# Kernel optimization log

Measured on AMD Instinct MI355X. Metric: run time of the kernel, lower is better.

Reference implementation:

```python
import jax, jax.numpy as jnp
import numpy as np

NUM_HEADS = 16
HIDDEN = 1024
TOTAL = 2048
NSEG = 8


def setup_inputs() -> dict:
    key = jax.random.key(0)
    ks = jax.random.split(key, 10)
    x = jax.random.normal(ks[0], (TOTAL, HIDDEN), dtype=jnp.float32)
    # cu_seqlens: [0, b1, ..., TOTAL], sorted segment boundaries
    inner = np.sort(np.random.default_rng(0).integers(1, TOTAL, size=NSEG - 1))
    cu_seqlens = jnp.asarray(np.concatenate([[0], inner, [TOTAL]]), dtype=jnp.int32)
    s = 1.0 / np.sqrt(HIDDEN)
    def lin(k):
        kw, kb = jax.random.split(k)
        W = jax.random.uniform(kw, (HIDDEN, HIDDEN), jnp.float32, -s, s)
        b = jax.random.uniform(kb, (HIDDEN,), jnp.float32, -s, s)
        return W, b
    Wq, bq = lin(ks[1]); Wk, bk = lin(ks[2]); Wv, bv = lin(ks[3]); Wo, bo = lin(ks[4])
    return {"hidden_states_packed": x, "cu_seqlens": cu_seqlens,
            "Wq": Wq, "bq": bq, "Wk": Wk, "bk": bk,
            "Wv": Wv, "bv": bv, "Wo": Wo, "bo": bo}


def reference(hidden_states_packed, cu_seqlens, Wq, bq, Wk, bk, Wv, bv, Wo, bo):
    T, H = hidden_states_packed.shape
    dh = H // NUM_HEADS
    x = hidden_states_packed
    q = (x @ Wq.T + bq).reshape(T, NUM_HEADS, dh)
    k = (x @ Wk.T + bk).reshape(T, NUM_HEADS, dh)
    v = (x @ Wv.T + bv).reshape(T, NUM_HEADS, dh)
    # segment id of each token from cu_seqlens boundaries
    seg = jnp.searchsorted(cu_seqlens, jnp.arange(T, dtype=jnp.int32), side="right")
    same_seg = seg[:, None] == seg[None, :]  # [T, T] block-diagonal mask
    scale = 1.0 / jnp.sqrt(jnp.asarray(dh, x.dtype))
    scores = jnp.einsum("qhd,khd->hqk", q, k) * scale  # [H, T, T]
    neg = jnp.asarray(jnp.finfo(scores.dtype).min, scores.dtype)
    scores = jnp.where(same_seg[None, :, :], scores, neg)
    attn = jax.nn.softmax(scores, axis=-1)
    ctx = jnp.einsum("hqk,khd->qhd", attn, v).reshape(T, H)
    return ctx @ Wo.T + bo
```

## Files before the change

kernel.cpp:

```cpp
#include <hip/hip_runtime.h>

typedef _Float16 f16x8 __attribute__((ext_vector_type(8)));
typedef _Float16 f16x4 __attribute__((ext_vector_type(4)));
typedef float    f32x4 __attribute__((ext_vector_type(4)));

#define MFMA_F16(a, b, c) __builtin_amdgcn_mfma_f32_16x16x32_f16((a), (b), (c), 0, 0, 0)

typedef __attribute__((address_space(1))) void gas_void;
typedef __attribute__((address_space(3))) void las_void;
#define GLOAD_LDS16(g, l) \
  __builtin_amdgcn_global_load_lds((gas_void*)(g), (las_void*)(l), 16, 0, 0)

#define NEG_INF (-__builtin_inff())

constexpr int T_SEQ  = 2048;
constexpr int HID    = 1024;
constexpr int NHEADS = 16;
constexpr int DH     = 64;
constexpr int NSEG   = 8;

__global__ __launch_bounds__(256) void convert_all(
    const float* __restrict__ x,
    const float* __restrict__ Wq, const float* __restrict__ Wk,
    const float* __restrict__ Wv, const float* __restrict__ Wo,
    _Float16* __restrict__ xh,
    _Float16* __restrict__ Wqh, _Float16* __restrict__ Wkh,
    _Float16* __restrict__ Wvh, _Float16* __restrict__ Woh) {
  int i = blockIdx.x * 256 + threadIdx.x;
  const float* src;
  _Float16* dst;
  int local;
  if (i < 524288) {
    src = x; dst = xh; local = i;
  } else {
    int j = i - 524288;
    int w = j >> 18;
    local = j & 262143;
    src = (w == 0) ? Wq : (w == 1) ? Wk : (w == 2) ? Wv : Wo;
    dst = (w == 0) ? Wqh : (w == 1) ? Wkh : (w == 2) ? Wvh : Woh;
  }
  float4 f = *(const float4*)(src + (size_t)local * 4);
  f16x4 h;
  h[0] = (_Float16)f.x; h[1] = (_Float16)f.y;
  h[2] = (_Float16)f.z; h[3] = (_Float16)f.w;
  *(f16x4*)(dst + (size_t)local * 4) = h;
}

template <int LAYOUT, int BM>
__device__ __forceinline__ void gemm128(const _Float16* __restrict__ A,
                                        const _Float16* __restrict__ B,
                                        const float* __restrict__ bias,
                                        _Float16* __restrict__ outh,
                                        float* __restrict__ outf) {
  constexpr int K = HID, N = HID;
  constexpr int MI = BM / 32;
  constexpr int LA = (BM * 8) / 512;
  __shared__ _Float16 As[BM * 64];
  __shared__ _Float16 Bs[128 * 64];
  const int tid  = threadIdx.x;
  const int wave = tid >> 6, lane = tid & 63;
  const int lr = lane & 15, lq = lane >> 4;
  const int wm = (wave >> 2) * (BM / 2);
  const int wn = (wave & 3) * 32;
  const int bm = blockIdx.y * BM, bn = blockIdx.x * 128;

  const _Float16* gA[LA > 0 ? LA : 1];
  const _Float16* gB[2];
  _Float16* lA[LA > 0 ? LA : 1];
  _Float16* lB[2];
#pragma unroll
  for (int i = 0; i < LA; ++i) {
    const int s = i * 512 + tid;
    const int row = s >> 3, pch = s & 7;
    const int lch = pch ^ (row & 7);
    gA[i] = A + (size_t)(bm + row) * K + lch * 8;
    lA[i] = &As[(i * 512 + wave * 64) * 8];
  }
#pragma unroll
  for (int i = 0; i < 2; ++i) {
    const int s = i * 512 + tid;
    const int row = s >> 3, pch = s & 7;
    const int lch = pch ^ (row & 7);
    gB[i] = B + (size_t)(bn + row) * K + lch * 8;
    lB[i] = &Bs[(i * 512 + wave * 64) * 8];
  }

  f32x4 acc[MI][2] = {};

  for (int kk = 0; kk < K; kk += 64) {
#pragma unroll
    for (int i = 0; i < LA; ++i) GLOAD_LDS16(gA[i] + kk, lA[i]);
#pragma unroll
    for (int i = 0; i < 2; ++i) GLOAD_LDS16(gB[i] + kk, lB[i]);
    __syncthreads();
#pragma unroll
    for (int ks = 0; ks < 2; ++ks) {
      f16x8 af[MI], bf[2];
#pragma unroll
      for (int mi = 0; mi < MI; ++mi) {
        const int row = wm + mi * 16 + lr;
        af[mi] = *(const f16x8*)&As[row * 64 + (((ks * 4 + lq) ^ (row & 7)) * 8)];
      }
#pragma unroll
      for (int ni = 0; ni < 2; ++ni) {
        const int row = wn + ni * 16 + lr;
        bf[ni] = *(const f16x8*)&Bs[row * 64 + (((ks * 4 + lq) ^ (row & 7)) * 8)];
      }
#pragma unroll
      for (int mi = 0; mi < MI; ++mi)
#pragma unroll
        for (int ni = 0; ni < 2; ++ni)
          acc[mi][ni] = MFMA_F16(af[mi], bf[ni], acc[mi][ni]);
    }
    __syncthreads();
  }

#pragma unroll
  for (int ni = 0; ni < 2; ++ni) {
    const int col = bn + wn + ni * 16 + lr;
    const float bv = bias[col];
#pragma unroll
    for (int mi = 0; mi < MI; ++mi) {
      const f32x4 v = acc[mi][ni];
      const int row0 = bm + wm + mi * 16 + lq * 4;
      if (LAYOUT == 3) {
        f16x4 o;
#pragma unroll
        for (int r = 0; r < 4; ++r) o[r] = (_Float16)(v[r] + bv);
        *(f16x4*)&outh[(size_t)col * T_SEQ + row0] = o;
      } else {
#pragma unroll
        for (int r = 0; r < 4; ++r) {
          const int row = row0 + r;
          const float val = v[r] + bv;
          if (LAYOUT == 0)
            outh[((size_t)(col >> 6) * T_SEQ + row) * DH + (col & 63)] = (_Float16)val;
          else
            outf[(size_t)row * N + col] = val;
        }
      }
    }
  }
}

__global__ __launch_bounds__(512) void gemm_qkv(
    const _Float16* __restrict__ xh,
    const _Float16* __restrict__ Wqh, const _Float16* __restrict__ Wkh,
    const _Float16* __restrict__ Wvh,
    const float* __restrict__ bq, const float* __restrict__ bk,
    const float* __restrict__ bv,
    _Float16* __restrict__ qp, _Float16* __restrict__ kp,
    _Float16* __restrict__ vT) {
  const int z = blockIdx.z;
  if (z == 0) {
    gemm128<0, 128>(xh, Wqh, bq, qp, nullptr);
  } else if (z == 1) {
    gemm128<0, 128>(xh, Wkh, bk, kp, nullptr);
  } else {
    gemm128<3, 128>(xh, Wvh, bv, vT, nullptr);
  }
}

__global__ __launch_bounds__(512) void gemm_out(
    const _Float16* __restrict__ ctxh, const _Float16* __restrict__ Woh,
    const float* __restrict__ bo, float* __restrict__ out) {
  gemm128<1, 64>(ctxh, Woh, bo, nullptr, out);
}

__device__ __forceinline__ float redsum16(float v) {
  v += __shfl_xor(v, 1);
  v += __shfl_xor(v, 2);
  v += __shfl_xor(v, 4);
  v += __shfl_xor(v, 8);
  return v;
}

__global__ __launch_bounds__(256, 2) void attn_kernel(
    const _Float16* __restrict__ qp, const _Float16* __restrict__ kp,
    const _Float16* __restrict__ vT, const int* __restrict__ cu,
    _Float16* __restrict__ ctx) {
  constexpr float SCL2E = 0.125f * 1.44269504f;
  constexpr int PSTR = 72;
  __shared__ _Float16 Pl[4 * 16 * PSTR];
  __shared__ float mO[2][16][64];
  __shared__ float mL[2][16];
  const int h  = blockIdx.y;
  const int q0 = blockIdx.x * 32;
  const int tid = threadIdx.x, wave = tid >> 6, lane = tid & 63;
  const int lr = lane & 15, lq = lane >> 4;
  const int qsub = wave & 1, khalf = wave >> 1;
  const int qw = q0 + qsub * 16;

  int cs[NSEG + 1];
#pragma unroll
  for (int i = 0; i <= NSEG; ++i) cs[i] = cu[i];

  int sstart[4], send[4];
#pragma unroll
  for (int r = 0; r < 4; ++r) {
    const int row = qw + lq * 4 + r;
    sstart[r] = 0; send[r] = T_SEQ;
#pragma unroll
    for (int s = 0; s < NSEG; ++s)
      if (row >= cs[s] && row < cs[s + 1]) { sstart[r] = cs[s]; send[r] = cs[s + 1]; }
  }
  int klo = 0, khi = T_SEQ;
#pragma unroll
  for (int s = 0; s < NSEG; ++s) {
    if (qw >= cs[s] && qw < cs[s + 1]) klo = cs[s];
    if (qw + 15 >= cs[s] && qw + 15 < cs[s + 1]) khi = cs[s + 1];
  }
  klo &= ~63;
  const int range = khi - klo;
  const int half = ((range + 127) >> 7) << 6;
  const int kstart = khalf ? (klo + half) : klo;
  int kend = khalf ? khi : (klo + half);
  kend = (kend < khi) ? kend : khi;

  const _Float16* qbase = qp + ((size_t)h * T_SEQ + qw + lr) * DH;
  const f16x8 qf0 = *(const f16x8*)(qbase + lq * 8);
  const f16x8 qf1 = *(const f16x8*)(qbase + 32 + lq * 8);

  const _Float16* kb = kp + (size_t)h * T_SEQ * DH;
  const _Float16* vb = vT + (size_t)h * DH * T_SEQ;

  float lst[4] = {0.f, 0.f, 0.f, 0.f};
  f32x4 oacc[4];
#pragma unroll
  for (int c = 0; c < 4; ++c) oacc[c] = f32x4{0.f, 0.f, 0.f, 0.f};

  _Float16* pw = &Pl[wave * 16 * PSTR];

  auto loadK = [&](int kt, f16x8 (&kf)[4][2]) {
#pragma unroll
    for (int n = 0; n < 4; ++n) {
      const int row = kt + n * 16 + lr;
      const _Float16* p = kb + (size_t)row * DH + lq * 8;
      kf[n][0] = *(const f16x8*)p;
      kf[n][1] = *(const f16x8*)(p + 32);
    }
  };
  auto loadV = [&](int kt, f16x8 (&vf)[4][2]) {
#pragma unroll
    for (int c = 0; c < 4; ++c) {
      const _Float16* p = vb + (size_t)(c * 16 + lr) * T_SEQ + kt + lq * 8;
      vf[c][0] = *(const f16x8*)p;
      vf[c][1] = *(const f16x8*)(p + 32);
    }
  };

  auto step = [&](int kt, f16x8 (&kf)[4][2], f16x8 (&vf)[4][2]) {
    f32x4 sc[4];
#pragma unroll
    for (int n = 0; n < 4; ++n) {
      sc[n] = f32x4{0.f, 0.f, 0.f, 0.f};
      sc[n] = MFMA_F16(qf0, kf[n][0], sc[n]);
      sc[n] = MFMA_F16(qf1, kf[n][1], sc[n]);
    }
#pragma unroll
    for (int r = 0; r < 4; ++r) {
      float p[4];
#pragma unroll
      for (int n = 0; n < 4; ++n) {
        const int col = kt + n * 16 + lr;
        const float vv =
            (col >= sstart[r] && col < send[r]) ? sc[n][r] * SCL2E : NEG_INF;
        p[n] = exp2f(vv);
      }
      lst[r] += (p[0] + p[1]) + (p[2] + p[3]);
      _Float16* pr = &pw[(lq * 4 + r) * PSTR + lr];
      pr[0]  = (_Float16)p[0];
      pr[16] = (_Float16)p[1];
      pr[32] = (_Float16)p[2];
      pr[48] = (_Float16)p[3];
    }
    const f16x8 pf0 = *(const f16x8*)&pw[lr * PSTR + lq * 8];
    const f16x8 pf1 = *(const f16x8*)&pw[lr * PSTR + 32 + lq * 8];
#pragma unroll
    for (int c = 0; c < 4; ++c) {
      oacc[c] = MFMA_F16(pf0, vf[c][0], oacc[c]);
      oacc[c] = MFMA_F16(pf1, vf[c][1], oacc[c]);
    }
  };

  if (kstart < kend) {
    f16x8 kA[4][2], vA[4][2], kB[4][2], vB[4][2];
    int kt = kstart;
    loadK(kt, kA);
    loadV(kt, vA);
    while (true) {
      if (kt + 64 < kend) { loadK(kt + 64, kB); loadV(kt + 64, vB); }
      step(kt, kA, vA);
      kt += 64;
      if (kt >= kend) break;
      if (kt + 64 < kend) { loadK(kt + 64, kA); loadV(kt + 64, vA); }
      step(kt, kB, vB);
      kt += 64;
      if (kt >= kend) break;
    }
  }

#pragma unroll
  for (int r = 0; r < 4; ++r) lst[r] = redsum16(lst[r]);

  if (khalf) {
#pragma unroll
    for (int c = 0; c < 4; ++c)
#pragma unroll
      for (int r = 0; r < 4; ++r)
        mO[qsub][lq * 4 + r][c * 16 + lr] = oacc[c][r];
    if (lr == 0) {
#pragma unroll
      for (int r = 0; r < 4; ++r) mL[qsub][lq * 4 + r] = lst[r];
    }
  }
  __syncthreads();
  if (!khalf) {
#pragma unroll
    for (int r = 0; r < 4; ++r) lst[r] += mL[qsub][lq * 4 + r];
#pragma unroll
    for (int c = 0; c < 4; ++c)
#pragma unroll
      for (int r = 0; r < 4; ++r) {
        const int row = qw + lq * 4 + r;
        const float val =
            (oacc[c][r] + mO[qsub][lq * 4 + r][c * 16 + lr]) / lst[r];
        ctx[(size_t)row * HID + h * DH + c * 16 + lr] = (_Float16)val;
      }
  }
}

extern "C" void kernel_launch(void* const* d_in, const int* in_sizes, int n_in,
                              void* d_out, int out_size, void* d_ws, size_t ws_size,
                              hipStream_t stream) {
  const float* x  = (const float*)d_in[0];
  const int* cu   = (const int*)d_in[1];
  const float* Wq = (const float*)d_in[2]; const float* bq = (const float*)d_in[3];
  const float* Wk = (const float*)d_in[4]; const float* bk = (const float*)d_in[5];
  const float* Wv = (const float*)d_in[6]; const float* bv = (const float*)d_in[7];
  const float* Wo = (const float*)d_in[8]; const float* bo = (const float*)d_in[9];
  float* out = (float*)d_out;

  char* ws = (char*)d_ws;
  _Float16* xh   = (_Float16*)(ws + (size_t)0);
  _Float16* Wqh  = (_Float16*)(ws + ((size_t)4 << 20));
  _Float16* Wkh  = (_Float16*)(ws + ((size_t)6 << 20));
  _Float16* Wvh  = (_Float16*)(ws + ((size_t)8 << 20));
  _Float16* Woh  = (_Float16*)(ws + ((size_t)10 << 20));
  _Float16* qp   = (_Float16*)(ws + ((size_t)12 << 20));
  _Float16* kp   = (_Float16*)(ws + ((size_t)16 << 20));
  _Float16* vT   = (_Float16*)(ws + ((size_t)20 << 20));
  _Float16* ctxh = (_Float16*)(ws + ((size_t)24 << 20));

  convert_all<<<6144, 256, 0, stream>>>(x, Wq, Wk, Wv, Wo, xh, Wqh, Wkh, Wvh, Woh);
  gemm_qkv<<<dim3(8, 16, 3), 512, 0, stream>>>(xh, Wqh, Wkh, Wvh, bq, bk, bv, qp, kp, vT);
  attn_kernel<<<dim3(T_SEQ / 32, NHEADS), 256, 0, stream>>>(qp, kp, vT, cu, ctxh);
  gemm_out<<<dim3(8, 32), 512, 0, stream>>>(ctxh, Woh, bo, out);
}
```

Baseline: 157.1 us.

## Share K/V tiles in LDS across four query waves per attention block

The attention kernel now handles 64 query rows per block using 8 waves: 4 query subtiles by 2 key halves. K and V tiles are loaded once into swizzled LDS with direct global-to-LDS loads and shared by the four query waves, instead of each wave loading its own K/V fragments into registers. This cuts redundant global/L2 traffic but adds two block barriers per step and drops the register double-buffering prefetch. The key range is now the union over 64 rows, which may add masked work at segment boundaries.

```diff
diff --git a/kernel.cpp b/kernel.cpp
--- a/kernel.cpp
+++ b/kernel.cpp
@@ -175,20 +175,22 @@
   return v;
 }
 
-__global__ __launch_bounds__(256, 2) void attn_kernel(
+__global__ __launch_bounds__(512, 4) void attn_kernel(
     const _Float16* __restrict__ qp, const _Float16* __restrict__ kp,
     const _Float16* __restrict__ vT, const int* __restrict__ cu,
     _Float16* __restrict__ ctx) {
   constexpr float SCL2E = 0.125f * 1.44269504f;
   constexpr int PSTR = 72;
-  __shared__ _Float16 Pl[4 * 16 * PSTR];
-  __shared__ float mO[2][16][64];
-  __shared__ float mL[2][16];
+  __shared__ _Float16 Ks[2][64 * 64];
+  __shared__ _Float16 Vs[2][64 * 64];
+  __shared__ _Float16 Pl[8][16 * PSTR];
+  __shared__ float mO[4][16][64];
+  __shared__ float mL[4][16];
   const int h  = blockIdx.y;
-  const int q0 = blockIdx.x * 32;
+  const int q0 = blockIdx.x * 64;
   const int tid = threadIdx.x, wave = tid >> 6, lane = tid & 63;
   const int lr = lane & 15, lq = lane >> 4;
-  const int qsub = wave & 1, khalf = wave >> 1;
+  const int qsub = wave & 3, khalf = wave >> 2;
   const int qw = q0 + qsub * 16;
 
   int cs[NSEG + 1];
@@ -207,15 +209,14 @@
   int klo = 0, khi = T_SEQ;
 #pragma unroll
   for (int s = 0; s < NSEG; ++s) {
-    if (qw >= cs[s] && qw < cs[s + 1]) klo = cs[s];
-    if (qw + 15 >= cs[s] && qw + 15 < cs[s + 1]) khi = cs[s + 1];
+    if (q0 >= cs[s] && q0 < cs[s + 1]) klo = cs[s];
+    if (q0 + 63 >= cs[s] && q0 + 63 < cs[s + 1]) khi = cs[s + 1];
   }
   klo &= ~63;
-  const int range = khi - klo;
-  const int half = ((range + 127) >> 7) << 6;
-  const int kstart = khalf ? (klo + half) : klo;
-  int kend = khalf ? khi : (klo + half);
-  kend = (kend < khi) ? kend : khi;
+  const int range  = khi - klo;
+  const int hlen   = ((range + 127) >> 7) << 6;
+  const int nsteps = hlen >> 6;
+  const int kstart = klo + khalf * hlen;
 
   const _Float16* qbase = qp + ((size_t)h * T_SEQ + qw + lr) * DH;
   const f16x8 qf0 = *(const f16x8*)(qbase + lq * 8);
@@ -224,38 +225,53 @@
   const _Float16* kb = kp + (size_t)h * T_SEQ * DH;
   const _Float16* vb = vT + (size_t)h * DH * T_SEQ;
 
+  const int ht = qsub * 64 + lane;
+  int kRow[2], kCol[2], vRow[2], vCol[2];
+  _Float16* lK[2];
+  _Float16* lV[2];
+#pragma unroll
+  for (int i = 0; i < 2; ++i) {
+    const int s = i * 256 + ht;
+    const int row = s >> 3, pch = s & 7;
+    const int lch = pch ^ (row & 7);
+    kRow[i] = row; kCol[i] = lch * 8;
+    vRow[i] = row; vCol[i] = lch * 8;
+    lK[i] = &Ks[khalf][(i * 256 + qsub * 64) * 8];
+    lV[i] = &Vs[khalf][(i * 256 + qsub * 64) * 8];
+  }
+
   float lst[4] = {0.f, 0.f, 0.f, 0.f};
   f32x4 oacc[4];
 #pragma unroll
   for (int c = 0; c < 4; ++c) oacc[c] = f32x4{0.f, 0.f, 0.f, 0.f};
 
-  _Float16* pw = &Pl[wave * 16 * PSTR];
-
-  auto loadK = [&](int kt, f16x8 (&kf)[4][2]) {
+  _Float16* pw = &Pl[wave][0];
+
+  for (int s = 0; s < nsteps; ++s) {
+    const int kt = kstart + s * 64;
+#pragma unroll
+    for (int i = 0; i < 2; ++i) {
+      const int grow = min(kt + kRow[i], T_SEQ - 1);
+      GLOAD_LDS16(kb + (size_t)grow * DH + kCol[i], lK[i]);
+    }
+#pragma unroll
+    for (int i = 0; i < 2; ++i) {
+      const int gcol = min(kt + vCol[i], T_SEQ - 8);
+      GLOAD_LDS16(vb + (size_t)vRow[i] * T_SEQ + gcol, lV[i]);
+    }
+    __syncthreads();
+
+    f32x4 sc[4];
 #pragma unroll
     for (int n = 0; n < 4; ++n) {
-      const int row = kt + n * 16 + lr;
-      const _Float16* p = kb + (size_t)row * DH + lq * 8;
-      kf[n][0] = *(const f16x8*)p;
-      kf[n][1] = *(const f16x8*)(p + 32);
-    }
-  };
-  auto loadV = [&](int kt, f16x8 (&vf)[4][2]) {
-#pragma unroll
-    for (int c = 0; c < 4; ++c) {
-      const _Float16* p = vb + (size_t)(c * 16 + lr) * T_SEQ + kt + lq * 8;
-      vf[c][0] = *(const f16x8*)p;
-      vf[c][1] = *(const f16x8*)(p + 32);
-    }
-  };
-
-  auto step = [&](int kt, f16x8 (&kf)[4][2], f16x8 (&vf)[4][2]) {
-    f32x4 sc[4];
-#pragma unroll
-    for (int n = 0; n < 4; ++n) {
+      const int row = n * 16 + lr;
+      const f16x8 kf0 =
+          *(const f16x8*)&Ks[khalf][row * 64 + (((0 * 4 + lq) ^ (row & 7)) * 8)];
+      const f16x8 kf1 =
+          *(const f16x8*)&Ks[khalf][row * 64 + (((1 * 4 + lq) ^ (row & 7)) * 8)];
       sc[n] = f32x4{0.f, 0.f, 0.f, 0.f};
-      sc[n] = MFMA_F16(qf0, kf[n][0], sc[n]);
-      sc[n] = MFMA_F16(qf1, kf[n][1], sc[n]);
+      sc[n] = MFMA_F16(qf0, kf0, sc[n]);
+      sc[n] = MFMA_F16(qf1, kf1, sc[n]);
     }
 #pragma unroll
     for (int r = 0; r < 4; ++r) {
@@ -278,26 +294,15 @@
     const f16x8 pf1 = *(const f16x8*)&pw[lr * PSTR + 32 + lq * 8];
 #pragma unroll
     for (int c = 0; c < 4; ++c) {
-      oacc[c] = MFMA_F16(pf0, vf[c][0], oacc[c]);
-      oacc[c] = MFMA_F16(pf1, vf[c][1], oacc[c]);
-    }
-  };
-
-  if (kstart < kend) {
-    f16x8 kA[4][2], vA[4][2], kB[4][2], vB[4][2];
-    int kt = kstart;
-    loadK(kt, kA);
-    loadV(kt, vA);
-    while (true) {
-      if (kt + 64 < kend) { loadK(kt + 64, kB); loadV(kt + 64, vB); }
-      step(kt, kA, vA);
-      kt += 64;
-      if (kt >= kend) break;
-      if (kt + 64 < kend) { loadK(kt + 64, kA); loadV(kt + 64, vA); }
-      step(kt, kB, vB);
-      kt += 64;
-      if (kt >= kend) break;
-    }
+      const int row = c * 16 + lr;
+      const f16x8 vf0 =
+          *(const f16x8*)&Vs[khalf][row * 64 + (((0 * 4 + lq) ^ (row & 7)) * 8)];
+      const f16x8 vf1 =
+          *(const f16x8*)&Vs[khalf][row * 64 + (((1 * 4 + lq) ^ (row & 7)) * 8)];
+      oacc[c] = MFMA_F16(pf0, vf0, oacc[c]);
+      oacc[c] = MFMA_F16(pf1, vf1, oacc[c]);
+    }
+    __syncthreads();
   }
 
 #pragma unroll
@@ -354,6 +359,6 @@
 
   convert_all<<<6144, 256, 0, stream>>>(x, Wq, Wk, Wv, Wo, xh, Wqh, Wkh, Wvh, Woh);
   gemm_qkv<<<dim3(8, 16, 3), 512, 0, stream>>>(xh, Wqh, Wkh, Wvh, bq, bk, bv, qp, kp, vT);
-  attn_kernel<<<dim3(T_SEQ / 32, NHEADS), 256, 0, stream>>>(qp, kp, vT, cu, ctxh);
+  attn_kernel<<<dim3(T_SEQ / 64, NHEADS), 512, 0, stream>>>(qp, kp, vT, cu, ctxh);
   gemm_out<<<dim3(8, 32), 512, 0, stream>>>(ctxh, Woh, bo, out);
 }
```

Result: faster. 141.7 us (-9.8%).
